# Kernel optimization log

Measured on AMD Instinct MI355X. Metric: run time of the kernel, lower is better.

## Reference

```python
import jax, jax.numpy as jnp
import numpy as np

NUM_DEPTH_BINS = 64
EPS = 1e-8


def bilinear_grid_sample(feats, grid):
    """torch.nn.functional.grid_sample, mode='bilinear', padding_mode='zeros',
    align_corners=False.  feats: [N, C, H, W]; grid: [N, Ho, Wo, 2] in [-1, 1].
    Returns [N, C, Ho, Wo]."""
    N, C, H, W = feats.shape
    x = (grid[..., 0] + 1.0) * (W * 0.5) - 0.5  # [N, Ho, Wo]
    y = (grid[..., 1] + 1.0) * (H * 0.5) - 0.5
    x0 = jnp.floor(x)
    y0 = jnp.floor(y)
    wx1 = x - x0
    wy1 = y - y0
    wx0 = 1.0 - wx1
    wy0 = 1.0 - wy1
    feats_flat = feats.reshape(N, C, H * W)

    def gather(ix, iy):
        valid = (ix >= 0) & (ix <= W - 1) & (iy >= 0) & (iy <= H - 1)
        ixc = jnp.clip(ix, 0, W - 1).astype(jnp.int32)
        iyc = jnp.clip(iy, 0, H - 1).astype(jnp.int32)
        idx = (iyc * W + ixc).reshape(N, 1, -1)  # [N,1,Ho*Wo]
        f = jnp.take_along_axis(feats_flat, idx, axis=2).reshape(N, C, *ix.shape[1:])
        return f * valid[:, None].astype(feats.dtype)

    out = (gather(x0, y0) * (wx0 * wy0)[:, None]
           + gather(x0 + 1, y0) * (wx1 * wy0)[:, None]
           + gather(x0, y0 + 1) * (wx0 * wy1)[:, None]
           + gather(x0 + 1, y0 + 1) * (wx1 * wy1)[:, None])
    return out


def _cost_volume(cur_feats, src_feats, src_extrinsics, src_Ks, cur_invK, min_depth, max_depth):
    B, K, C, H, W = src_feats.shape
    D = NUM_DEPTH_BINS
    # log-spaced depth planes, shape [B, D, 1, 1]
    ramp = jnp.linspace(0.0, 1.0, D).reshape(1, D, 1, 1).astype(cur_feats.dtype)
    depth_planes_bd11 = jnp.exp(jnp.log(min_depth) + jnp.log(max_depth / min_depth) * ramp)
    # BackprojectDepth: half-pixel-centered homogeneous pixel coords [3, N]
    xs, ys = jnp.meshgrid(jnp.arange(W, dtype=cur_feats.dtype) + 0.5,
                          jnp.arange(H, dtype=cur_feats.dtype) + 0.5)
    pix_3n = jnp.stack([xs.ravel(), ys.ravel(), jnp.ones(H * W, cur_feats.dtype)])
    cam_dirs_b3n = jnp.einsum('bij,jn->bin', cur_invK[:, :3, :3], pix_3n)
    world_bd3n = depth_planes_bd11.reshape(B, D, 1, 1) * cam_dirs_b3n[:, None]  # [B,D,3,N]
    world_bd4n = jnp.concatenate(
        [world_bd3n, jnp.ones((B, D, 1, H * W), world_bd3n.dtype)], axis=2)
    # Project3D: P = K @ extrinsics, project, perspective divide
    P_bk34 = jnp.einsum('bkij,bkjl->bkil', src_Ks, src_extrinsics)[:, :, :3]
    cam_bkd3n = jnp.einsum('bkij,bdjn->bkdin', P_bk34, world_bd4n)  # [B,K,D,3,N]
    z_bkdn = cam_bkd3n[:, :, :, 2]
    pix_bkd2n = cam_bkd3n[:, :, :, :2] / (z_bkdn[:, :, :, None] + EPS)
    # uv = 2 * pix * (1/W, 1/H) - 1
    u = 2.0 * pix_bkd2n[:, :, :, 0] / W - 1.0
    v = 2.0 * pix_bkd2n[:, :, :, 1] / H - 1.0
    grid = jnp.stack([u, v], axis=-1).reshape(B * K, D * H, W, 2)
    warped = bilinear_grid_sample(src_feats.reshape(B * K, C, H, W), grid)
    warped = warped.reshape(B, K, C, D, H, W)
    mask = (z_bkdn > 0).astype(cur_feats.dtype).reshape(B, K, D, H, W)
    # channel dot product with current features, masked, summed over views
    dots_bkdhw = jnp.einsum('bkcdhw,bchw->bkdhw', warped, cur_feats) * mask
    cost_volume_bdhw = dots_bkdhw.sum(axis=1)
    return cost_volume_bdhw


def setup_inputs() -> dict:
    key = jax.random.key(0)
    B, K, C, H, W = 1, 7, 16, 96, 128
    k1, k2 = jax.random.split(key)
    cur_feats = jax.random.normal(k1, (B, C, H, W), jnp.float32)
    src_feats = jax.random.normal(k2, (B, K, C, H, W), jnp.float32)
    rng = np.random.default_rng(0)
    fx = 0.8 * W
    Kmat = np.array([[fx, 0, W / 2, 0], [0, fx, H / 2, 0],
                     [0, 0, 1, 0], [0, 0, 0, 1]], np.float32)

    def small_pose():
        aa = rng.normal(size=3) * 0.05
        th = np.linalg.norm(aa)
        ax = aa / (th + 1e-12)
        Kx = np.array([[0, -ax[2], ax[1]], [ax[2], 0, -ax[0]], [-ax[1], ax[0], 0]])
        R = np.eye(3) + np.sin(th) * Kx + (1 - np.cos(th)) * (Kx @ Kx)
        T = np.eye(4, dtype=np.float64)
        T[:3, :3] = R
        T[:3, 3] = rng.normal(size=3) * 0.08
        return T

    src_extrinsics = np.stack([[small_pose() for _ in range(K)] for _ in range(B)])
    src_poses = np.linalg.inv(src_extrinsics)
    return {
        'cur_feats': cur_feats,
        'src_feats': src_feats,
        'src_extrinsics': jnp.asarray(src_extrinsics, jnp.float32),
        'src_poses': jnp.asarray(src_poses, jnp.float32),
        'src_Ks': jnp.asarray(np.broadcast_to(Kmat, (B, K, 4, 4)).copy()),
        'cur_invK': jnp.asarray(np.broadcast_to(np.linalg.inv(Kmat), (B, 4, 4)).astype(np.float32).copy()),
        'min_depth': jnp.full((B, 1, 1, 1), 0.25, jnp.float32),
        'max_depth': jnp.full((B, 1, 1, 1), 5.0, jnp.float32),
    }


def reference(cur_feats, src_feats, src_extrinsics, src_poses, src_Ks, cur_invK, min_depth, max_depth):
    del src_poses  # unused, matching the original (del src_poses)
    return _cost_volume(cur_feats, src_feats, src_extrinsics, src_Ks, cur_invK, min_depth, max_depth)
```

## Files before the change

kernel.cpp:

```cpp
#include <hip/hip_runtime.h>

#define CV_H 96
#define CV_W 128
#define CV_C 16
#define CV_K 7
#define CV_D 64
#define CV_EPS 1e-8f
#define CV_HW (CV_H * CV_W)

typedef _Float16 v2h __attribute__((ext_vector_type(2)));
typedef _Float16 v8h __attribute__((ext_vector_type(8)));

#if __has_builtin(__builtin_amdgcn_fdot2)
#define FDOT2(a, b, c) __builtin_amdgcn_fdot2((a), (b), (c), false)
#else
#define FDOT2(a, b, c) ((float)(a)[0] * (float)(b)[0] + (float)(a)[1] * (float)(b)[1] + (c))
#endif

__global__ __launch_bounds__(256) void cv_prep(
    const float* __restrict__ cur, const float* __restrict__ src,
    const float* __restrict__ extr, const float* __restrict__ Ks,
    const float* __restrict__ invK, const float* __restrict__ minD,
    const float* __restrict__ maxD,
    float* __restrict__ depths, float* __restrict__ M,
    _Float16* __restrict__ srcT, _Float16* __restrict__ curT) {
    const int b = blockIdx.x;
    if (b == (CV_K + 1) * CV_H) {
        int t = threadIdx.x;
        if (t < CV_D) {
            float mn = minD[0], mx = maxD[0];
            float ramp = (float)t * (1.0f / (CV_D - 1));
            depths[t] = expf(logf(mn) + logf(mx / mn) * ramp);
        }
        if (t < CV_K) {
            const float* Km = Ks + t * 16;
            const float* E  = extr + t * 16;
            float P[3][4];
            for (int i = 0; i < 3; ++i)
                for (int j = 0; j < 4; ++j) {
                    float s = 0.f;
                    for (int l = 0; l < 4; ++l) s += Km[i * 4 + l] * E[l * 4 + j];
                    P[i][j] = s;
                }
            float* Mk = M + t * 12;
            for (int i = 0; i < 3; ++i)
                for (int j = 0; j < 3; ++j) {
                    float s = 0.f;
                    for (int l = 0; l < 3; ++l) s += P[i][l] * invK[l * 4 + j];
                    Mk[i * 3 + j] = s;
                }
            for (int i = 0; i < 3; ++i) Mk[9 + i] = P[i][3];
        }
        return;
    }
    const int g = b / CV_H;
    const int h = b % CV_H;
    const float* rowBase = (g < CV_K) ? (src + (size_t)g * CV_C * CV_HW + h * CV_W)
                                      : (cur + h * CV_W);
    __shared__ float lds[CV_C][CV_W + 2];
    const int t = threadIdx.x;
#pragma unroll
    for (int i = 0; i < 2; ++i) {
        int f  = t + i * 256;
        int c  = f >> 5;
        int w4 = (f & 31) << 2;
        float4 v = *(const float4*)(rowBase + (size_t)c * CV_HW + w4);
        lds[c][w4 + 0] = v.x; lds[c][w4 + 1] = v.y;
        lds[c][w4 + 2] = v.z; lds[c][w4 + 3] = v.w;
    }
    __syncthreads();
    const int p  = t >> 1;
    const int cb = (t & 1) << 3;
    v8h o;
#pragma unroll
    for (int j = 0; j < 8; ++j) o[j] = (_Float16)lds[cb + j][p];
    _Float16* dst = (g < CV_K)
        ? (srcT + ((size_t)g * CV_HW + h * CV_W + p) * CV_C + cb)
        : (curT + ((size_t)h * CV_W + p) * CV_C + cb);
    *(v8h*)dst = o;
}

__device__ __forceinline__ float dot16h(v8h a0, v8h a1, v8h b0, v8h b1) {
    const v2h* pa0 = (const v2h*)&a0; const v2h* pb0 = (const v2h*)&b0;
    const v2h* pa1 = (const v2h*)&a1; const v2h* pb1 = (const v2h*)&b1;
    float s = 0.f;
#pragma unroll
    for (int i = 0; i < 4; ++i) s = FDOT2(pa0[i], pb0[i], s);
#pragma unroll
    for (int i = 0; i < 4; ++i) s = FDOT2(pa1[i], pb1[i], s);
    return s;
}

__global__ __launch_bounds__(256, 2) void cv_main(
    const _Float16* __restrict__ srcT,
    const _Float16* __restrict__ curT,
    const float* __restrict__ depths,
    const float* __restrict__ Mg,
    float* __restrict__ out) {
    const int bx  = blockIdx.x;
    const int rem = bx % 192;
    const int db2 = bx / 192;
    const int t   = threadIdx.x;
    const int wx = t & 7, hy = (t >> 3) & 7, dd = t >> 6;
    const int w = (rem & 15) * 8 + wx;
    const int h = (rem >> 4) * 8 + hy;
    const int dbase = db2 * 16 + dd * 4;

    const float px = w + 0.5f;
    const float py = h + 0.5f;
    float dpt[4];
#pragma unroll
    for (int j = 0; j < 4; ++j) dpt[j] = depths[dbase + j];

    const v8h* cp = (const v8h*)(curT + (h * CV_W + w) * CV_C);
    const v8h c0 = cp[0], c1 = cp[1];

    float acc[4] = {0.f, 0.f, 0.f, 0.f};
#pragma unroll
    for (int k = 0; k < CV_K; ++k) {
        const float* Mk = Mg + k * 12;
        const float qx = Mk[0] * px + Mk[1] * py + Mk[2];
        const float qy = Mk[3] * px + Mk[4] * py + Mk[5];
        const float qz = Mk[6] * px + Mk[7] * py + Mk[8];
        const float bxk = Mk[9], byk = Mk[10], bzk = Mk[11];
        const v8h* base = (const v8h*)srcT + (size_t)k * (CV_HW * 2);

        int o00[4], o10[4], o01[4], o11[4];
        float w00[4], w10[4], w01[4], w11[4], vld[4];
#pragma unroll
        for (int j = 0; j < 4; ++j) {
            float depth = dpt[j];
            float cx = fmaf(depth, qx, bxk);
            float cy = fmaf(depth, qy, byk);
            float cz = fmaf(depth, qz, bzk);
            vld[j] = (cz > 0.f) ? 1.f : 0.f;
            float inv = __builtin_amdgcn_rcpf(fabsf(cz) + CV_EPS);
            float x = fminf(fmaxf(fmaf(cx, inv, -0.5f), -4.0f), (float)(CV_W + 3));
            float y = fminf(fmaxf(fmaf(cy, inv, -0.5f), -4.0f), (float)(CV_H + 3));
            float xf = floorf(x), yf = floorf(y);
            float wx1 = x - xf, wy1 = y - yf;
            float wx0 = 1.f - wx1, wy0 = 1.f - wy1;
            int x0 = (int)xf, y0 = (int)yf;
            int x1 = x0 + 1, y1 = y0 + 1;
            bool vx0 = (unsigned)x0 < (unsigned)CV_W;
            bool vx1 = (unsigned)x1 < (unsigned)CV_W;
            bool vy0 = (unsigned)y0 < (unsigned)CV_H;
            bool vy1 = (unsigned)y1 < (unsigned)CV_H;
            int cx0 = min(max(x0, 0), CV_W - 1);
            int cx1 = min(max(x1, 0), CV_W - 1);
            int cy0 = min(max(y0, 0), CV_H - 1) * (CV_W * 2);
            int cy1 = min(max(y1, 0), CV_H - 1) * (CV_W * 2);
            o00[j] = cy0 + cx0 * 2; o10[j] = cy0 + cx1 * 2;
            o01[j] = cy1 + cx0 * 2; o11[j] = cy1 + cx1 * 2;
            w00[j] = (vx0 && vy0) ? wx0 * wy0 : 0.f;
            w10[j] = (vx1 && vy0) ? wx1 * wy0 : 0.f;
            w01[j] = (vx0 && vy1) ? wx0 * wy1 : 0.f;
            w11[j] = (vx1 && vy1) ? wx1 * wy1 : 0.f;
        }

#pragma unroll
        for (int jp = 0; jp < 2; ++jp) {
            const int j0 = jp * 2, j1 = jp * 2 + 1;
            v8h A00 = base[o00[j0]/2*2];
            v8h B00 = base[o00[j0] + 1 - 1 + 1];
            (void)A00; (void)B00;
            v8h a00 = base[o00[j0]],     b00 = base[o00[j0] + 1];
            v8h a10 = base[o10[j0]],     b10 = base[o10[j0] + 1];
            v8h a01 = base[o01[j0]],     b01 = base[o01[j0] + 1];
            v8h a11 = base[o11[j0]],     b11 = base[o11[j0] + 1];
            v8h e00 = base[o00[j1]],     f00 = base[o00[j1] + 1];
            v8h e10 = base[o10[j1]],     f10 = base[o10[j1] + 1];
            v8h e01 = base[o01[j1]],     f01 = base[o01[j1] + 1];
            v8h e11 = base[o11[j1]],     f11 = base[o11[j1] + 1];
            float s0 = w00[j0] * dot16h(a00, b00, c0, c1)
                     + w10[j0] * dot16h(a10, b10, c0, c1)
                     + w01[j0] * dot16h(a01, b01, c0, c1)
                     + w11[j0] * dot16h(a11, b11, c0, c1);
            float s1 = w00[j1] * dot16h(e00, f00, c0, c1)
                     + w10[j1] * dot16h(e10, f10, c0, c1)
                     + w01[j1] * dot16h(e01, f01, c0, c1)
                     + w11[j1] * dot16h(e11, f11, c0, c1);
            acc[j0] = fmaf(vld[j0], s0, acc[j0]);
            acc[j1] = fmaf(vld[j1], s1, acc[j1]);
        }
    }
#pragma unroll
    for (int j = 0; j < 4; ++j)
        out[((dbase + j) * CV_H + h) * CV_W + w] = acc[j];
}

extern "C" void kernel_launch(void* const* d_in, const int* in_sizes, int n_in,
                              void* d_out, int out_size, void* d_ws, size_t ws_size,
                              hipStream_t stream) {
    const float* cur_feats = (const float*)d_in[0];
    const float* src_feats = (const float*)d_in[1];
    const float* extr      = (const float*)d_in[2];
    const float* Ks        = (const float*)d_in[4];
    const float* invK      = (const float*)d_in[5];
    const float* minD      = (const float*)d_in[6];
    const float* maxD      = (const float*)d_in[7];
    float* out = (float*)d_out;

    float* wsf    = (float*)d_ws;
    float* depths = wsf;
    float* M      = wsf + 64;
    _Float16* srcT = (_Float16*)(wsf + 256);
    _Float16* curT = srcT + (size_t)CV_K * CV_HW * CV_C;

    cv_prep<<<(CV_K + 1) * CV_H + 1, 256, 0, stream>>>(
        cur_feats, src_feats, extr, Ks, invK, minD, maxD, depths, M, srcT, curT);

    cv_main<<<(CV_D / 16) * (CV_H / 8) * (CV_W / 8), 256, 0, stream>>>(
        srcT, curT, depths, M, out);
}
```

Measured before the change: 33.47 us.

## Stage projected source footprint in LDS per view before bilinear gathers

For each source view, the block projects the corners of its 8x8 pixel by 16-depth tile to bound the sampled source region. It cooperatively copies that region of fp16 source features into shared memory and gathers the bilinear taps from LDS instead of global memory. A global-memory path is kept when the footprint is too large or the depth is invalid. This adds barriers, a serialized view loop (unroll 1) and up to 40KB of LDS per block, which may reduce occupancy and overlap between views.

```diff
diff --git a/kernel.cpp b/kernel.cpp
--- a/kernel.cpp
+++ b/kernel.cpp
@@ -7,6 +7,7 @@
 #define CV_D 64
 #define CV_EPS 1e-8f
 #define CV_HW (CV_H * CV_W)
+#define LDS_V8H 2560
 
 typedef _Float16 v2h __attribute__((ext_vector_type(2)));
 typedef _Float16 v8h __attribute__((ext_vector_type(8)));
@@ -97,13 +98,14 @@
     const float* __restrict__ depths,
     const float* __restrict__ Mg,
     float* __restrict__ out) {
+    __shared__ v8h tile[LDS_V8H];
     const int bx  = blockIdx.x;
     const int rem = bx % 192;
     const int db2 = bx / 192;
     const int t   = threadIdx.x;
     const int wx = t & 7, hy = (t >> 3) & 7, dd = t >> 6;
-    const int w = (rem & 15) * 8 + wx;
-    const int h = (rem >> 4) * 8 + hy;
+    const int w0 = (rem & 15) * 8, h0 = (rem >> 4) * 8;
+    const int w = w0 + wx, h = h0 + hy;
     const int dbase = db2 * 16 + dd * 4;
 
     const float px = w + 0.5f;
@@ -111,21 +113,68 @@
     float dpt[4];
 #pragma unroll
     for (int j = 0; j < 4; ++j) dpt[j] = depths[dbase + j];
+    const float d_lo = depths[db2 * 16], d_hi = depths[db2 * 16 + 15];
 
     const v8h* cp = (const v8h*)(curT + (h * CV_W + w) * CV_C);
     const v8h c0 = cp[0], c1 = cp[1];
 
     float acc[4] = {0.f, 0.f, 0.f, 0.f};
-#pragma unroll
+#pragma unroll 1
     for (int k = 0; k < CV_K; ++k) {
         const float* Mk = Mg + k * 12;
         const float qx = Mk[0] * px + Mk[1] * py + Mk[2];
         const float qy = Mk[3] * px + Mk[4] * py + Mk[5];
         const float qz = Mk[6] * px + Mk[7] * py + Mk[8];
         const float bxk = Mk[9], byk = Mk[10], bzk = Mk[11];
-        const v8h* base = (const v8h*)srcT + (size_t)k * (CV_HW * 2);
-
-        int o00[4], o10[4], o01[4], o11[4];
+        const v8h* sv = (const v8h*)srcT + (size_t)k * (CV_HW * 2);
+
+        float umin = 1e30f, umax = -1e30f, vmin = 1e30f, vmax = -1e30f;
+        float czmin = 1e30f;
+#pragma unroll
+        for (int ci = 0; ci < 8; ++ci) {
+            float cpx = (ci & 1) ? (w0 + 7.5f) : (w0 + 0.5f);
+            float cpy = (ci & 2) ? (h0 + 7.5f) : (h0 + 0.5f);
+            float dc  = (ci & 4) ? d_hi : d_lo;
+            float ccx = fmaf(dc, Mk[0] * cpx + Mk[1] * cpy + Mk[2], bxk);
+            float ccy = fmaf(dc, Mk[3] * cpx + Mk[4] * cpy + Mk[5], byk);
+            float ccz = fmaf(dc, Mk[6] * cpx + Mk[7] * cpy + Mk[8], bzk);
+            czmin = fminf(czmin, ccz);
+            float ri = __builtin_amdgcn_rcpf(fmaxf(ccz, 1e-8f));
+            float cu = fmaf(ccx, ri, -0.5f);
+            float cv = fmaf(ccy, ri, -0.5f);
+            umin = fminf(umin, cu); umax = fmaxf(umax, cu);
+            vmin = fminf(vmin, cv); vmax = fmaxf(vmax, cv);
+        }
+        umin = fminf(fmaxf(umin, -2.0f), 200.0f);
+        umax = fminf(fmaxf(umax, -2.0f), 200.0f);
+        vmin = fminf(fmaxf(vmin, -2.0f), 200.0f);
+        vmax = fminf(fmaxf(vmax, -2.0f), 200.0f);
+        const int ox  = max(0, (int)floorf(umin) - 1);
+        const int xhi = min(CV_W - 1, (int)floorf(umax) + 2);
+        const int oy  = max(0, (int)floorf(vmin) - 1);
+        const int yhi = min(CV_H - 1, (int)floorf(vmax) + 2);
+        const int Wp = xhi - ox + 1, Hp = yhi - oy + 1;
+        const int pitch = Wp * 2 + 1;
+        const bool ok = (czmin > 1e-6f) && (Wp > 0) && (Hp > 0) &&
+                        (Hp * pitch <= LDS_V8H);
+
+        __syncthreads();
+        if (ok) {
+            const int nch = Wp * 2;
+            for (int r = (t >> 6); r < Hp; r += 4) {
+                const v8h* grow = sv + ((oy + r) * CV_W + ox) * 2;
+                v8h* lrow = tile + r * pitch;
+                for (int q = (t & 63); q < nch; q += 64)
+                    lrow[q] = grow[q];
+            }
+            __syncthreads();
+        }
+        const int bxlo = ok ? ox : 0,  bxhi = ok ? xhi : CV_W - 1;
+        const int bylo = ok ? oy : 0,  byhi = ok ? yhi : CV_H - 1;
+        const int rp   = ok ? pitch : CV_W * 2;
+        const int obase = bylo * rp + bxlo * 2;
+
+        int i00[4], i10[4], i01[4], i11[4];
         float w00[4], w10[4], w01[4], w11[4], vld[4];
 #pragma unroll
         for (int j = 0; j < 4; ++j) {
@@ -146,42 +195,44 @@
             bool vx1 = (unsigned)x1 < (unsigned)CV_W;
             bool vy0 = (unsigned)y0 < (unsigned)CV_H;
             bool vy1 = (unsigned)y1 < (unsigned)CV_H;
-            int cx0 = min(max(x0, 0), CV_W - 1);
-            int cx1 = min(max(x1, 0), CV_W - 1);
-            int cy0 = min(max(y0, 0), CV_H - 1) * (CV_W * 2);
-            int cy1 = min(max(y1, 0), CV_H - 1) * (CV_W * 2);
-            o00[j] = cy0 + cx0 * 2; o10[j] = cy0 + cx1 * 2;
-            o01[j] = cy1 + cx0 * 2; o11[j] = cy1 + cx1 * 2;
+            int cx0 = min(max(x0, bxlo), bxhi);
+            int cx1 = min(max(x1, bxlo), bxhi);
+            int r0 = min(max(y0, bylo), byhi) * rp - obase;
+            int r1 = min(max(y1, bylo), byhi) * rp - obase;
+            i00[j] = r0 + cx0 * 2; i10[j] = r0 + cx1 * 2;
+            i01[j] = r1 + cx0 * 2; i11[j] = r1 + cx1 * 2;
             w00[j] = (vx0 && vy0) ? wx0 * wy0 : 0.f;
             w10[j] = (vx1 && vy0) ? wx1 * wy0 : 0.f;
             w01[j] = (vx0 && vy1) ? wx0 * wy1 : 0.f;
             w11[j] = (vx1 && vy1) ? wx1 * wy1 : 0.f;
         }
 
-#pragma unroll
-        for (int jp = 0; jp < 2; ++jp) {
-            const int j0 = jp * 2, j1 = jp * 2 + 1;
-            v8h A00 = base[o00[j0]/2*2];
-            v8h B00 = base[o00[j0] + 1 - 1 + 1];
-            (void)A00; (void)B00;
-            v8h a00 = base[o00[j0]],     b00 = base[o00[j0] + 1];
-            v8h a10 = base[o10[j0]],     b10 = base[o10[j0] + 1];
-            v8h a01 = base[o01[j0]],     b01 = base[o01[j0] + 1];
-            v8h a11 = base[o11[j0]],     b11 = base[o11[j0] + 1];
-            v8h e00 = base[o00[j1]],     f00 = base[o00[j1] + 1];
-            v8h e10 = base[o10[j1]],     f10 = base[o10[j1] + 1];
-            v8h e01 = base[o01[j1]],     f01 = base[o01[j1] + 1];
-            v8h e11 = base[o11[j1]],     f11 = base[o11[j1] + 1];
-            float s0 = w00[j0] * dot16h(a00, b00, c0, c1)
-                     + w10[j0] * dot16h(a10, b10, c0, c1)
-                     + w01[j0] * dot16h(a01, b01, c0, c1)
-                     + w11[j0] * dot16h(a11, b11, c0, c1);
-            float s1 = w00[j1] * dot16h(e00, f00, c0, c1)
-                     + w10[j1] * dot16h(e10, f10, c0, c1)
-                     + w01[j1] * dot16h(e01, f01, c0, c1)
-                     + w11[j1] * dot16h(e11, f11, c0, c1);
-            acc[j0] = fmaf(vld[j0], s0, acc[j0]);
-            acc[j1] = fmaf(vld[j1], s1, acc[j1]);
+        if (ok) {
+#pragma unroll
+            for (int j = 0; j < 4; ++j) {
+                v8h a00 = tile[i00[j]], b00 = tile[i00[j] + 1];
+                v8h a10 = tile[i10[j]], b10 = tile[i10[j] + 1];
+                v8h a01 = tile[i01[j]], b01 = tile[i01[j] + 1];
+                v8h a11 = tile[i11[j]], b11 = tile[i11[j] + 1];
+                float s = w00[j] * dot16h(a00, b00, c0, c1)
+                        + w10[j] * dot16h(a10, b10, c0, c1)
+                        + w01[j] * dot16h(a01, b01, c0, c1)
+                        + w11[j] * dot16h(a11, b11, c0, c1);
+                acc[j] = fmaf(vld[j], s, acc[j]);
+            }
+        } else {
+#pragma unroll
+            for (int j = 0; j < 4; ++j) {
+                v8h a00 = sv[i00[j]], b00 = sv[i00[j] + 1];
+                v8h a10 = sv[i10[j]], b10 = sv[i10[j] + 1];
+                v8h a01 = sv[i01[j]], b01 = sv[i01[j] + 1];
+                v8h a11 = sv[i11[j]], b11 = sv[i11[j] + 1];
+                float s = w00[j] * dot16h(a00, b00, c0, c1)
+                        + w10[j] * dot16h(a10, b10, c0, c1)
+                        + w01[j] * dot16h(a01, b01, c0, c1)
+                        + w11[j] * dot16h(a11, b11, c0, c1);
+                acc[j] = fmaf(vld[j], s, acc[j]);
+            }
         }
     }
 #pragma unroll
```

Result: slower. 39.11 us (+16.8%).
